# Kernel tuning notes

Measured on AMD Instinct MI355X. Metric: run time of the kernel, lower is better.

## Reference

```python
import jax, jax.numpy as jnp
import numpy as np

N_NODES = 50000
N_EDGES = 800000
IN_C = 128
HID = 128
OUT_C = 64
N_GRAPHS = 256


def setup_inputs() -> dict:
    key = jax.random.key(0)
    ks = jax.random.split(key, 12)
    x = jax.random.normal(ks[0], (N_NODES, IN_C), dtype=jnp.float32)
    edge_index = jax.random.randint(ks[1], (2, N_EDGES), 0, N_NODES, dtype=jnp.int32)
    batch = jnp.sort(jax.random.randint(ks[2], (N_NODES,), 0, N_GRAPHS, dtype=jnp.int32))
    def lin(k, fan_in, fan_out):
        bound = 1.0 / np.sqrt(fan_in)
        kw, kb = jax.random.split(k)
        W = jax.random.uniform(kw, (fan_in, fan_out), minval=-bound, maxval=bound, dtype=jnp.float32)
        b = jax.random.uniform(kb, (fan_out,), minval=-bound, maxval=bound, dtype=jnp.float32)
        return W, b
    W1a, b1a = lin(ks[3], IN_C, HID)
    W1b, b1b = lin(ks[4], HID, HID)
    W2a, b2a = lin(ks[5], HID, HID)
    W2b, b2b = lin(ks[6], HID, HID)
    Wl, bl = lin(ks[7], HID, OUT_C)
    return {"x": x, "edge_index": edge_index, "batch": batch,
            "W1a": W1a, "b1a": b1a, "W1b": W1b, "b1b": b1b,
            "W2a": W2a, "b2a": b2a, "W2b": W2b, "b2b": b2b,
            "Wl": Wl, "bl": bl}


def gin_conv(x, edge_index, Wa, ba, Wb, bb):
    # GINConv with eps=0: h_i = MLP(x_i + sum_{j->i} x_j)
    src, dst = edge_index[0], edge_index[1]
    agg = jax.ops.segment_sum(x[src], dst, num_segments=x.shape[0])  # [N, d]
    h = x + agg
    h = jax.nn.relu(h @ Wa + ba) @ Wb + bb
    return h


def reference(x, edge_index, batch, W1a, b1a, W1b, b1b, W2a, b2a, W2b, b2b, Wl, bl):
    h = gin_conv(x, edge_index, W1a, b1a, W1b, b1b)
    h = gin_conv(h, edge_index, W2a, b2a, W2b, b2b)
    # global mean pool over graphs in the batch
    sums = jax.ops.segment_sum(h, batch, num_segments=N_GRAPHS)          # [G, HID]
    cnts = jax.ops.segment_sum(jnp.ones((h.shape[0],), h.dtype), batch, num_segments=N_GRAPHS)
    pooled = sums / jnp.maximum(cnts, 1.0)[:, None]
    return pooled @ Wl + bl  # [G, OUT_C]
```

## Files before the change

kernel.cpp:

```cpp
#include <hip/hip_runtime.h>

constexpr int N  = 50000;
constexpr int E  = 800000;
constexpr int C  = 128;
constexpr int G  = 256;
constexpr int OC = 64;
constexpr int D  = 64;

constexpr int NBUCK = 196;
constexpr int BCAP  = 5120;
constexpr int EB = (E + 4095) / 4096;
constexpr int WB = 256;
constexpr int XB = (N * C / 8 + 255) / 256;

typedef __attribute__((ext_vector_type(8))) short short8;
typedef __attribute__((ext_vector_type(4))) float f32x4;
typedef __attribute__((ext_vector_type(2))) float f32x2;

__device__ __forceinline__ unsigned int au(float f) { return __float_as_uint(f); }

__device__ __forceinline__ unsigned short f2bf(float f) {
    unsigned int u = au(f);
    u += 0x7fffu + ((u >> 16) & 1u);
    return (unsigned short)(u >> 16);
}
__device__ __forceinline__ unsigned int pack_bf16(float lo, float hi) {
    return ((au(hi) + 0x8000u) & 0xFFFF0000u) | ((au(lo) + 0x8000u) >> 16);
}

__device__ __forceinline__ void acc16(f32x2* a, uint4 v) {
    a[0] += __builtin_amdgcn_cvt_pk_f32_fp8((int)v.x, false);
    a[1] += __builtin_amdgcn_cvt_pk_f32_fp8((int)v.x, true);
    a[2] += __builtin_amdgcn_cvt_pk_f32_fp8((int)v.y, false);
    a[3] += __builtin_amdgcn_cvt_pk_f32_fp8((int)v.y, true);
    a[4] += __builtin_amdgcn_cvt_pk_f32_fp8((int)v.z, false);
    a[5] += __builtin_amdgcn_cvt_pk_f32_fp8((int)v.z, true);
    a[6] += __builtin_amdgcn_cvt_pk_f32_fp8((int)v.w, false);
    a[7] += __builtin_amdgcn_cvt_pk_f32_fp8((int)v.w, true);
}
__device__ __forceinline__ void set16(f32x2* a, uint4 v) {
    a[0] = __builtin_amdgcn_cvt_pk_f32_fp8((int)v.x, false);
    a[1] = __builtin_amdgcn_cvt_pk_f32_fp8((int)v.x, true);
    a[2] = __builtin_amdgcn_cvt_pk_f32_fp8((int)v.y, false);
    a[3] = __builtin_amdgcn_cvt_pk_f32_fp8((int)v.y, true);
    a[4] = __builtin_amdgcn_cvt_pk_f32_fp8((int)v.z, false);
    a[5] = __builtin_amdgcn_cvt_pk_f32_fp8((int)v.z, true);
    a[6] = __builtin_amdgcn_cvt_pk_f32_fp8((int)v.w, false);
    a[7] = __builtin_amdgcn_cvt_pk_f32_fp8((int)v.w, true);
}


__global__ __launch_bounds__(256) void build_prep_kernel(const int* __restrict__ src,
                                                         const int* __restrict__ dst,
                                                         int* __restrict__ bcount,
                                                         unsigned int* __restrict__ bucketbuf,
                                                         const float* __restrict__ W1a,
                                                         const float* __restrict__ W1b,
                                                         const float* __restrict__ W2a,
                                                         const float* __restrict__ W2b,
                                                         const float* __restrict__ x,
                                                         unsigned short* __restrict__ wt,
                                                         unsigned int* __restrict__ x8) {
    int b = blockIdx.x;
    if (b < EB) {
        __shared__ int lcount[NBUCK];
        __shared__ int lbase[NBUCK];
        __shared__ int lcur[NBUCK];
        int tid = threadIdx.x;
        for (int i = tid; i < NBUCK; i += 256) { lcount[i] = 0; lcur[i] = 0; }
        __syncthreads();
        int e0 = b * 4096;
        int sv[16], dv[16];
#pragma unroll
        for (int i = 0; i < 16; ++i) {
            int e = e0 + i * 256 + tid;
            if (e < E) {
                sv[i] = src[e];
                dv[i] = dst[e];
                atomicAdd(&lcount[dv[i] >> 8], 1);
            } else {
                dv[i] = -1;
            }
        }
        __syncthreads();
        if (tid < NBUCK) {
            int c = lcount[tid];
            lbase[tid] = (c > 0) ? atomicAdd(&bcount[tid], c) : 0;
        }
        __syncthreads();
#pragma unroll
        for (int i = 0; i < 16; ++i) {
            if (dv[i] >= 0) {
                int bk = dv[i] >> 8;
                int pos = lbase[bk] + atomicAdd(&lcur[bk], 1);
                if (pos < BCAP)
                    bucketbuf[(size_t)bk * BCAP + pos] =
                        ((unsigned int)sv[i] << 16) | (unsigned int)(dv[i] & 255);
            }
        }
    } else if (b < EB + WB) {
        const float* Ws[4] = {W1a, W1b, W2a, W2b};
        int idx = (b - EB) * 256 + threadIdx.x;
        int which = idx >> 14;
        int el    = idx & 16383;
        int n = el >> 7, k = el & 127;
        wt[idx] = f2bf(Ws[which][k * 128 + n]);
    } else {
        int idx = (b - EB - WB) * 256 + threadIdx.x;
        const float4* x4 = (const float4*)x;
        float4 v0 = x4[idx * 2];
        float4 v1 = x4[idx * 2 + 1];
        unsigned int lo = 0, hi = 0;
        lo = (unsigned int)__builtin_amdgcn_cvt_pk_fp8_f32(v0.x, v0.y, (int)lo, false);
        lo = (unsigned int)__builtin_amdgcn_cvt_pk_fp8_f32(v0.z, v0.w, (int)lo, true);
        hi = (unsigned int)__builtin_amdgcn_cvt_pk_fp8_f32(v1.x, v1.y, (int)hi, false);
        hi = (unsigned int)__builtin_amdgcn_cvt_pk_fp8_f32(v1.z, v1.w, (int)hi, true);
        ((uint2*)x8)[idx] = make_uint2(lo, hi);
    }
}


__global__ __launch_bounds__(256) void bucket_fill_kernel(const int* __restrict__ bcount,
                                                          const unsigned int* __restrict__ bucketbuf,
                                                          unsigned short* __restrict__ ell,
                                                          int* __restrict__ deg) {
    __shared__ int lcur[256];
    int b = blockIdx.x;
    int tid = threadIdx.x;
    lcur[tid] = 0;
    __syncthreads();
    int cnt = min(bcount[b], BCAP);
    const unsigned int* buf = bucketbuf + (size_t)b * BCAP;
    int nbase = b << 8;
    for (int i = tid; i < cnt; i += 256) {
        unsigned int e = buf[i];
        int dlow = (int)(e & 255u);
        int s = (int)(e >> 16);
        int p = atomicAdd(&lcur[dlow], 1);
        if (p < D) ell[(size_t)p * N + nbase + dlow] = (unsigned short)s;
    }
    __syncthreads();
    int node = nbase + tid;
    if (node < N) deg[node] = lcur[tid];
}


__global__ __launch_bounds__(256) void aggregate_kernel(const unsigned char* __restrict__ Fg,
                                                        const int* __restrict__ deg,
                                                        const unsigned short* __restrict__ ell,
                                                        unsigned short* __restrict__ Y) {
    int grp = threadIdx.x >> 3;
    int l   = threadIdx.x & 7;
    int n = blockIdx.x * 32 + grp;
    if (n >= N) return;
    const uint4* F16 = (const uint4*)Fg;
    f32x2 a[8];
    int dg = min(deg[n], D);
    const unsigned short* ecol = ell + n;
    set16(a, F16[(size_t)n * 8 + l]);
    int j = 0;
    if (dg >= 8) {
        int i0 = ecol[0];
        int i1 = ecol[(size_t)1 * N];
        int i2 = ecol[(size_t)2 * N];
        int i3 = ecol[(size_t)3 * N];
        int i4 = ecol[(size_t)4 * N];
        int i5 = ecol[(size_t)5 * N];
        int i6 = ecol[(size_t)6 * N];
        int i7 = ecol[(size_t)7 * N];
        uint4 v0 = F16[(size_t)i0 * 8 + l];
        uint4 v1 = F16[(size_t)i1 * 8 + l];
        uint4 v2 = F16[(size_t)i2 * 8 + l];
        uint4 v3 = F16[(size_t)i3 * 8 + l];
        uint4 v4 = F16[(size_t)i4 * 8 + l];
        uint4 v5 = F16[(size_t)i5 * 8 + l];
        uint4 v6 = F16[(size_t)i6 * 8 + l];
        uint4 v7 = F16[(size_t)i7 * 8 + l];
        for (j = 8; j + 8 <= dg; j += 8) {
            int t0 = ecol[(size_t)(j + 0) * N];
            int t1 = ecol[(size_t)(j + 1) * N];
            int t2 = ecol[(size_t)(j + 2) * N];
            int t3 = ecol[(size_t)(j + 3) * N];
            int t4 = ecol[(size_t)(j + 4) * N];
            int t5 = ecol[(size_t)(j + 5) * N];
            int t6 = ecol[(size_t)(j + 6) * N];
            int t7 = ecol[(size_t)(j + 7) * N];
            uint4 w0 = F16[(size_t)t0 * 8 + l];
            uint4 w1 = F16[(size_t)t1 * 8 + l];
            uint4 w2 = F16[(size_t)t2 * 8 + l];
            uint4 w3 = F16[(size_t)t3 * 8 + l];
            uint4 w4 = F16[(size_t)t4 * 8 + l];
            uint4 w5 = F16[(size_t)t5 * 8 + l];
            uint4 w6 = F16[(size_t)t6 * 8 + l];
            uint4 w7 = F16[(size_t)t7 * 8 + l];
            acc16(a, v0); acc16(a, v1); acc16(a, v2); acc16(a, v3);
            acc16(a, v4); acc16(a, v5); acc16(a, v6); acc16(a, v7);
            v0 = w0; v1 = w1; v2 = w2; v3 = w3;
            v4 = w4; v5 = w5; v6 = w6; v7 = w7;
        }
        acc16(a, v0); acc16(a, v1); acc16(a, v2); acc16(a, v3);
        acc16(a, v4); acc16(a, v5); acc16(a, v6); acc16(a, v7);
    }
    for (; j < dg; ++j) {
        uint4 v = F16[(size_t)ecol[(size_t)j * N] * 8 + l];
        acc16(a, v);
    }
    uint4 o0, o1;
    o0.x = pack_bf16(a[0].x, a[0].y); o0.y = pack_bf16(a[1].x, a[1].y);
    o0.z = pack_bf16(a[2].x, a[2].y); o0.w = pack_bf16(a[3].x, a[3].y);
    o1.x = pack_bf16(a[4].x, a[4].y); o1.y = pack_bf16(a[5].x, a[5].y);
    o1.z = pack_bf16(a[6].x, a[6].y); o1.w = pack_bf16(a[7].x, a[7].y);
    uint4* yp = (uint4*)(Y + (size_t)n * 128 + l * 16);
    yp[0] = o0;
    yp[1] = o1;
}


__global__ __launch_bounds__(256) void mlp_kernel(const unsigned short* __restrict__ Xg,
                                                  const unsigned short* __restrict__ WaT,
                                                  const float* __restrict__ ba,
                                                  const unsigned short* __restrict__ WbT,
                                                  const float* __restrict__ bb,
                                                  unsigned char* __restrict__ Hg8,
                                                  unsigned short* __restrict__ Hgb,
                                                  int outFp8) {
    constexpr int LD = 136;
    __shared__ short Xl[64 * LD];
    __shared__ short Wl[128 * LD];
    int tid  = threadIdx.x;
    int lane = tid & 63;
    int wave = tid >> 6;
    int row0 = blockIdx.x * 64;

    const short8* Xg8 = (const short8*)(Xg + (size_t)row0 * 128);
#pragma unroll
    for (int i = tid; i < 1024; i += 256) {
        int r = i >> 4, c = i & 15;
        *((short8*)(Xl + r * LD) + c) = Xg8[i];
    }
    const short8* Wa8 = (const short8*)WaT;
#pragma unroll
    for (int i = tid; i < 2048; i += 256) {
        int r = i >> 4, c = i & 15;
        *((short8*)(Wl + r * LD) + c) = Wa8[i];
    }

    int mw = wave >> 1, nw = wave & 1;
    int lid = lane & 15, quad = lane >> 4;

    f32x4 acc[2][4];
#pragma unroll
    for (int nt = 0; nt < 4; ++nt) {
        float b = ba[nw * 64 + nt * 16 + lid];
        acc[0][nt] = (f32x4){b, b, b, b};
        acc[1][nt] = (f32x4){b, b, b, b};
    }
    __syncthreads();

#pragma unroll
    for (int ks = 0; ks < 4; ++ks) {
        short8 a0 = *(const short8*)(Xl + (mw * 32 + lid) * LD + ks * 32 + quad * 8);
        short8 a1 = *(const short8*)(Xl + (mw * 32 + 16 + lid) * LD + ks * 32 + quad * 8);
#pragma unroll
        for (int nt = 0; nt < 4; ++nt) {
            short8 bf = *(const short8*)(Wl + (nw * 64 + nt * 16 + lid) * LD + ks * 32 + quad * 8);
            acc[0][nt] = __builtin_amdgcn_mfma_f32_16x16x32_bf16(a0, bf, acc[0][nt], 0, 0, 0);
            acc[1][nt] = __builtin_amdgcn_mfma_f32_16x16x32_bf16(a1, bf, acc[1][nt], 0, 0, 0);
        }
    }
    __syncthreads();

#pragma unroll
    for (int mt = 0; mt < 2; ++mt) {
#pragma unroll
        for (int nt = 0; nt < 4; ++nt) {
            int mbase = mw * 32 + mt * 16 + quad * 4;
            int n = nw * 64 + nt * 16 + lid;
            f32x4 v = acc[mt][nt];
#pragma unroll
            for (int r = 0; r < 4; ++r)
                Xl[(mbase + r) * LD + n] = (short)f2bf(fmaxf(v[r], 0.f));
        }
    }
    const short8* Wb8 = (const short8*)WbT;
#pragma unroll
    for (int i = tid; i < 2048; i += 256) {
        int r = i >> 4, c = i & 15;
        *((short8*)(Wl + r * LD) + c) = Wb8[i];
    }
    f32x4 acc2[2][4];
#pragma unroll
    for (int nt = 0; nt < 4; ++nt) {
        float b = bb[nw * 64 + nt * 16 + lid];
        acc2[0][nt] = (f32x4){b, b, b, b};
        acc2[1][nt] = (f32x4){b, b, b, b};
    }
    __syncthreads();

#pragma unroll
    for (int ks = 0; ks < 4; ++ks) {
        short8 a0 = *(const short8*)(Xl + (mw * 32 + lid) * LD + ks * 32 + quad * 8);
        short8 a1 = *(const short8*)(Xl + (mw * 32 + 16 + lid) * LD + ks * 32 + quad * 8);
#pragma unroll
        for (int nt = 0; nt < 4; ++nt) {
            short8 bf = *(const short8*)(Wl + (nw * 64 + nt * 16 + lid) * LD + ks * 32 + quad * 8);
            acc2[0][nt] = __builtin_amdgcn_mfma_f32_16x16x32_bf16(a0, bf, acc2[0][nt], 0, 0, 0);
            acc2[1][nt] = __builtin_amdgcn_mfma_f32_16x16x32_bf16(a1, bf, acc2[1][nt], 0, 0, 0);
        }
    }

#pragma unroll
    for (int mt = 0; mt < 2; ++mt) {
#pragma unroll
        for (int nt = 0; nt < 4; ++nt) {
            int mbase = row0 + mw * 32 + mt * 16 + quad * 4;
            int n = nw * 64 + nt * 16 + lid;
            f32x4 v = acc2[mt][nt];
            if (outFp8) {
#pragma unroll
                for (int r = 0; r < 4; ++r) {
                    int row = mbase + r;
                    if (row < N) {
                        unsigned int p = (unsigned int)__builtin_amdgcn_cvt_pk_fp8_f32(v[r], 0.f, 0, false);
                        Hg8[(size_t)row * 128 + n] = (unsigned char)(p & 0xFF);
                    }
                }
            } else {
#pragma unroll
                for (int r = 0; r < 4; ++r) {
                    int row = mbase + r;
                    if (row < N) Hgb[(size_t)row * 128 + n] = f2bf(v[r]);
                }
            }
        }
    }
}


__global__ __launch_bounds__(256) void pool_partial_kernel(const unsigned short* __restrict__ H,
                                                           const int* __restrict__ batch,
                                                           float* __restrict__ gsum,
                                                           int* __restrict__ gcnt) {
    int tid = threadIdx.x;
    int w = tid >> 6;
    int l = tid & 63;
    int r0 = blockIdx.x * 64 + w * 16;
    if (r0 >= N) return;
    int rend = min(r0 + 16, N);
    const unsigned int* H2 = (const unsigned int*)H;
    int curg = batch[r0];
    int runstart = r0;
    float a0 = 0.f, a1 = 0.f;
    for (int r = r0; r < rend; ++r) {
        int g = batch[r];
        if (g != curg) {
            atomicAdd(&gsum[curg * C + 2 * l], a0);
            atomicAdd(&gsum[curg * C + 2 * l + 1], a1);
            if (l == 0) atomicAdd(&gcnt[curg], r - runstart);
            curg = g; runstart = r; a0 = 0.f; a1 = 0.f;
        }
        unsigned int v = H2[(size_t)r * 64 + l];
        a0 += __uint_as_float((v & 0xffffu) << 16);
        a1 += __uint_as_float(v & 0xffff0000u);
    }
    atomicAdd(&gsum[curg * C + 2 * l], a0);
    atomicAdd(&gsum[curg * C + 2 * l + 1], a1);
    if (l == 0) atomicAdd(&gcnt[curg], rend - runstart);
}


__global__ __launch_bounds__(64) void head_kernel(const float* __restrict__ gsum,
                                                  const int* __restrict__ gcnt,
                                                  const float* __restrict__ Wl,
                                                  const float* __restrict__ bl,
                                                  float* __restrict__ out) {
    int g = blockIdx.x;
    int t = threadIdx.x;
    __shared__ float pooled[C];
    float inv = 1.0f / (float)max(gcnt[g], 1);
    pooled[t]      = gsum[g * C + t] * inv;
    pooled[t + 64] = gsum[g * C + 64 + t] * inv;
    __syncthreads();
    float o = bl[t];
#pragma unroll 4
    for (int k = 0; k < C; ++k) o += pooled[k] * Wl[k * OC + t];
    out[g * OC + t] = o;
}


extern "C" void kernel_launch(void* const* d_in, const int* in_sizes, int n_in,
                              void* d_out, int out_size, void* d_ws, size_t ws_size,
                              hipStream_t stream) {
    const float* x    = (const float*)d_in[0];
    const int*   ei   = (const int*)d_in[1];
    const int*   bat  = (const int*)d_in[2];
    const float* W1a  = (const float*)d_in[3];
    const float* b1a  = (const float*)d_in[4];
    const float* W1b  = (const float*)d_in[5];
    const float* b1b  = (const float*)d_in[6];
    const float* W2a  = (const float*)d_in[7];
    const float* b2a  = (const float*)d_in[8];
    const float* W2b  = (const float*)d_in[9];
    const float* b2b  = (const float*)d_in[10];
    const float* Wl   = (const float*)d_in[11];
    const float* bl   = (const float*)d_in[12];
    float*       out  = (float*)d_out;

    float* gsum    = (float*)d_ws;
    int*   gcnt    = (int*)(gsum + G * C);
    int*   bcount  = gcnt + G;
    int*   deg     = bcount + NBUCK;
    unsigned int* bucketbuf = (unsigned int*)(deg + N);
    unsigned short* ell = (unsigned short*)(bucketbuf + (size_t)NBUCK * BCAP);
    unsigned short* wt  = ell + (size_t)N * D;
    unsigned char*  x8  = (unsigned char*)(wt + 4 * 16384);
    unsigned char*  h8  = x8 + (size_t)N * 128;
    unsigned short* y   = (unsigned short*)(h8 + (size_t)N * 128);
    unsigned short* hb  = y + (size_t)(N + 64) * 128;

    const unsigned short* wt1a = wt;
    const unsigned short* wt1b = wt + 16384;
    const unsigned short* wt2a = wt + 2 * 16384;
    const unsigned short* wt2b = wt + 3 * 16384;

    const int* src = ei;
    const int* dst = ei + E;

    hipMemsetAsync(gsum, 0, (size_t)(G * C + G + NBUCK) * sizeof(int), stream);

    build_prep_kernel<<<EB + WB + XB, 256, 0, stream>>>(src, dst, bcount, bucketbuf,
                                                        W1a, W1b, W2a, W2b, x,
                                                        wt, (unsigned int*)x8);
    bucket_fill_kernel<<<NBUCK, 256, 0, stream>>>(bcount, bucketbuf, ell, deg);

    int ab = (N + 31) / 32;
    int mb = (N + 63) / 64;

    aggregate_kernel<<<ab, 256, 0, stream>>>(x8, deg, ell, y);
    mlp_kernel<<<mb, 256, 0, stream>>>(y, wt1a, b1a, wt1b, b1b, h8, nullptr, 1);

    aggregate_kernel<<<ab, 256, 0, stream>>>(h8, deg, ell, y);
    mlp_kernel<<<mb, 256, 0, stream>>>(y, wt2a, b2a, wt2b, b2b, nullptr, hb, 0);

    pool_partial_kernel<<<mb, 256, 0, stream>>>(hb, bat, gsum, gcnt);
    head_kernel<<<G, 64, 0, stream>>>(gsum, gcnt, Wl, bl, out);
}
```

Measured before the change: 222.1 us.

## Fuse aggregation, MLP and mean-pool partial sums into one conv kernel

Merges the gather-sum aggregation into the MLP kernel so each block aggregates its 64 rows straight into shared memory, removing the bf16 intermediate round trip through global memory and two launches. The second conv's epilogue accumulates pooled sums with atomics directly instead of writing hidden states, and graph counts move into the prep kernel via a shared-memory histogram. The cost is lower occupancy and latency hiding for the gather phase, since it now shares a block with large LDS tiles, and more global atomics in the epilogue.

```diff
diff --git a/kernel.cpp b/kernel.cpp
--- a/kernel.cpp
+++ b/kernel.cpp
@@ -12,6 +12,7 @@
 constexpr int EB = (E + 4095) / 4096;
 constexpr int WB = 256;
 constexpr int XB = (N * C / 8 + 255) / 256;
+constexpr int GB = (N + 255) / 256;
 
 typedef __attribute__((ext_vector_type(8))) short short8;
 typedef __attribute__((ext_vector_type(4))) float f32x4;
@@ -60,7 +61,9 @@
                                                          const float* __restrict__ W2b,
                                                          const float* __restrict__ x,
                                                          unsigned short* __restrict__ wt,
-                                                         unsigned int* __restrict__ x8) {
+                                                         unsigned int* __restrict__ x8,
+                                                         const int* __restrict__ batch,
+                                                         int* __restrict__ gcnt) {
     int b = blockIdx.x;
     if (b < EB) {
         __shared__ int lcount[NBUCK];
@@ -105,7 +108,7 @@
         int el    = idx & 16383;
         int n = el >> 7, k = el & 127;
         wt[idx] = f2bf(Ws[which][k * 128 + n]);
-    } else {
+    } else if (b < EB + WB + XB) {
         int idx = (b - EB - WB) * 256 + threadIdx.x;
         const float4* x4 = (const float4*)x;
         float4 v0 = x4[idx * 2];
@@ -116,6 +119,16 @@
         hi = (unsigned int)__builtin_amdgcn_cvt_pk_fp8_f32(v1.x, v1.y, (int)hi, false);
         hi = (unsigned int)__builtin_amdgcn_cvt_pk_fp8_f32(v1.z, v1.w, (int)hi, true);
         ((uint2*)x8)[idx] = make_uint2(lo, hi);
+    } else {
+        __shared__ int h[G];
+        int tid = threadIdx.x;
+        h[tid] = 0;
+        __syncthreads();
+        int i = (b - EB - WB - XB) * 256 + tid;
+        if (i < N) atomicAdd(&h[batch[i]], 1);
+        __syncthreads();
+        int c = h[tid];
+        if (c > 0) atomicAdd(&gcnt[tid], c);
     }
 }
 
@@ -145,85 +158,17 @@
 }
 
 
-__global__ __launch_bounds__(256) void aggregate_kernel(const unsigned char* __restrict__ Fg,
-                                                        const int* __restrict__ deg,
-                                                        const unsigned short* __restrict__ ell,
-                                                        unsigned short* __restrict__ Y) {
-    int grp = threadIdx.x >> 3;
-    int l   = threadIdx.x & 7;
-    int n = blockIdx.x * 32 + grp;
-    if (n >= N) return;
-    const uint4* F16 = (const uint4*)Fg;
-    f32x2 a[8];
-    int dg = min(deg[n], D);
-    const unsigned short* ecol = ell + n;
-    set16(a, F16[(size_t)n * 8 + l]);
-    int j = 0;
-    if (dg >= 8) {
-        int i0 = ecol[0];
-        int i1 = ecol[(size_t)1 * N];
-        int i2 = ecol[(size_t)2 * N];
-        int i3 = ecol[(size_t)3 * N];
-        int i4 = ecol[(size_t)4 * N];
-        int i5 = ecol[(size_t)5 * N];
-        int i6 = ecol[(size_t)6 * N];
-        int i7 = ecol[(size_t)7 * N];
-        uint4 v0 = F16[(size_t)i0 * 8 + l];
-        uint4 v1 = F16[(size_t)i1 * 8 + l];
-        uint4 v2 = F16[(size_t)i2 * 8 + l];
-        uint4 v3 = F16[(size_t)i3 * 8 + l];
-        uint4 v4 = F16[(size_t)i4 * 8 + l];
-        uint4 v5 = F16[(size_t)i5 * 8 + l];
-        uint4 v6 = F16[(size_t)i6 * 8 + l];
-        uint4 v7 = F16[(size_t)i7 * 8 + l];
-        for (j = 8; j + 8 <= dg; j += 8) {
-            int t0 = ecol[(size_t)(j + 0) * N];
-            int t1 = ecol[(size_t)(j + 1) * N];
-            int t2 = ecol[(size_t)(j + 2) * N];
-            int t3 = ecol[(size_t)(j + 3) * N];
-            int t4 = ecol[(size_t)(j + 4) * N];
-            int t5 = ecol[(size_t)(j + 5) * N];
-            int t6 = ecol[(size_t)(j + 6) * N];
-            int t7 = ecol[(size_t)(j + 7) * N];
-            uint4 w0 = F16[(size_t)t0 * 8 + l];
-            uint4 w1 = F16[(size_t)t1 * 8 + l];
-            uint4 w2 = F16[(size_t)t2 * 8 + l];
-            uint4 w3 = F16[(size_t)t3 * 8 + l];
-            uint4 w4 = F16[(size_t)t4 * 8 + l];
-            uint4 w5 = F16[(size_t)t5 * 8 + l];
-            uint4 w6 = F16[(size_t)t6 * 8 + l];
-            uint4 w7 = F16[(size_t)t7 * 8 + l];
-            acc16(a, v0); acc16(a, v1); acc16(a, v2); acc16(a, v3);
-            acc16(a, v4); acc16(a, v5); acc16(a, v6); acc16(a, v7);
-            v0 = w0; v1 = w1; v2 = w2; v3 = w3;
-            v4 = w4; v5 = w5; v6 = w6; v7 = w7;
-        }
-        acc16(a, v0); acc16(a, v1); acc16(a, v2); acc16(a, v3);
-        acc16(a, v4); acc16(a, v5); acc16(a, v6); acc16(a, v7);
-    }
-    for (; j < dg; ++j) {
-        uint4 v = F16[(size_t)ecol[(size_t)j * N] * 8 + l];
-        acc16(a, v);
-    }
-    uint4 o0, o1;
-    o0.x = pack_bf16(a[0].x, a[0].y); o0.y = pack_bf16(a[1].x, a[1].y);
-    o0.z = pack_bf16(a[2].x, a[2].y); o0.w = pack_bf16(a[3].x, a[3].y);
-    o1.x = pack_bf16(a[4].x, a[4].y); o1.y = pack_bf16(a[5].x, a[5].y);
-    o1.z = pack_bf16(a[6].x, a[6].y); o1.w = pack_bf16(a[7].x, a[7].y);
-    uint4* yp = (uint4*)(Y + (size_t)n * 128 + l * 16);
-    yp[0] = o0;
-    yp[1] = o1;
-}
-
-
-__global__ __launch_bounds__(256) void mlp_kernel(const unsigned short* __restrict__ Xg,
-                                                  const unsigned short* __restrict__ WaT,
-                                                  const float* __restrict__ ba,
-                                                  const unsigned short* __restrict__ WbT,
-                                                  const float* __restrict__ bb,
-                                                  unsigned char* __restrict__ Hg8,
-                                                  unsigned short* __restrict__ Hgb,
-                                                  int outFp8) {
+__global__ __launch_bounds__(256) void conv_kernel(const unsigned char* __restrict__ Fg,
+                                                   const int* __restrict__ deg,
+                                                   const unsigned short* __restrict__ ell,
+                                                   const unsigned short* __restrict__ WaT,
+                                                   const float* __restrict__ ba,
+                                                   const unsigned short* __restrict__ WbT,
+                                                   const float* __restrict__ bb,
+                                                   unsigned char* __restrict__ Hg8,
+                                                   const int* __restrict__ batch,
+                                                   float* __restrict__ gsum,
+                                                   int outFp8) {
     constexpr int LD = 136;
     __shared__ short Xl[64 * LD];
     __shared__ short Wl[128 * LD];
@@ -232,17 +177,86 @@
     int wave = tid >> 6;
     int row0 = blockIdx.x * 64;
 
-    const short8* Xg8 = (const short8*)(Xg + (size_t)row0 * 128);
-#pragma unroll
-    for (int i = tid; i < 1024; i += 256) {
-        int r = i >> 4, c = i & 15;
-        *((short8*)(Xl + r * LD) + c) = Xg8[i];
-    }
     const short8* Wa8 = (const short8*)WaT;
 #pragma unroll
     for (int i = tid; i < 2048; i += 256) {
         int r = i >> 4, c = i & 15;
         *((short8*)(Wl + r * LD) + c) = Wa8[i];
+    }
+
+    {
+        int grp = tid >> 3;
+        int l   = tid & 7;
+        const uint4* F16 = (const uint4*)Fg;
+#pragma unroll 1
+        for (int pass = 0; pass < 2; ++pass) {
+            int lr = pass * 32 + grp;
+            int n  = row0 + lr;
+            f32x2 a[8];
+            if (n < N) {
+                int dg = min(deg[n], D);
+                const unsigned short* ecol = ell + n;
+                set16(a, F16[(size_t)n * 8 + l]);
+                int j = 0;
+                if (dg >= 8) {
+                    int i0 = ecol[0];
+                    int i1 = ecol[(size_t)1 * N];
+                    int i2 = ecol[(size_t)2 * N];
+                    int i3 = ecol[(size_t)3 * N];
+                    int i4 = ecol[(size_t)4 * N];
+                    int i5 = ecol[(size_t)5 * N];
+                    int i6 = ecol[(size_t)6 * N];
+                    int i7 = ecol[(size_t)7 * N];
+                    uint4 v0 = F16[(size_t)i0 * 8 + l];
+                    uint4 v1 = F16[(size_t)i1 * 8 + l];
+                    uint4 v2 = F16[(size_t)i2 * 8 + l];
+                    uint4 v3 = F16[(size_t)i3 * 8 + l];
+                    uint4 v4 = F16[(size_t)i4 * 8 + l];
+                    uint4 v5 = F16[(size_t)i5 * 8 + l];
+                    uint4 v6 = F16[(size_t)i6 * 8 + l];
+                    uint4 v7 = F16[(size_t)i7 * 8 + l];
+                    for (j = 8; j + 8 <= dg; j += 8) {
+                        int t0 = ecol[(size_t)(j + 0) * N];
+                        int t1 = ecol[(size_t)(j + 1) * N];
+                        int t2 = ecol[(size_t)(j + 2) * N];
+                        int t3 = ecol[(size_t)(j + 3) * N];
+                        int t4 = ecol[(size_t)(j + 4) * N];
+                        int t5 = ecol[(size_t)(j + 5) * N];
+                        int t6 = ecol[(size_t)(j + 6) * N];
+                        int t7 = ecol[(size_t)(j + 7) * N];
+                        uint4 w0 = F16[(size_t)t0 * 8 + l];
+                        uint4 w1 = F16[(size_t)t1 * 8 + l];
+                        uint4 w2 = F16[(size_t)t2 * 8 + l];
+                        uint4 w3 = F16[(size_t)t3 * 8 + l];
+                        uint4 w4 = F16[(size_t)t4 * 8 + l];
+                        uint4 w5 = F16[(size_t)t5 * 8 + l];
+                        uint4 w6 = F16[(size_t)t6 * 8 + l];
+                        uint4 w7 = F16[(size_t)t7 * 8 + l];
+                        acc16(a, v0); acc16(a, v1); acc16(a, v2); acc16(a, v3);
+                        acc16(a, v4); acc16(a, v5); acc16(a, v6); acc16(a, v7);
+                        v0 = w0; v1 = w1; v2 = w2; v3 = w3;
+                        v4 = w4; v5 = w5; v6 = w6; v7 = w7;
+                    }
+                    acc16(a, v0); acc16(a, v1); acc16(a, v2); acc16(a, v3);
+                    acc16(a, v4); acc16(a, v5); acc16(a, v6); acc16(a, v7);
+                }
+                for (; j < dg; ++j) {
+                    uint4 v = F16[(size_t)ecol[(size_t)j * N] * 8 + l];
+                    acc16(a, v);
+                }
+            } else {
+#pragma unroll
+                for (int q = 0; q < 8; ++q) a[q] = (f32x2){0.f, 0.f};
+            }
+            uint4 o0, o1;
+            o0.x = pack_bf16(a[0].x, a[0].y); o0.y = pack_bf16(a[1].x, a[1].y);
+            o0.z = pack_bf16(a[2].x, a[2].y); o0.w = pack_bf16(a[3].x, a[3].y);
+            o1.x = pack_bf16(a[4].x, a[4].y); o1.y = pack_bf16(a[5].x, a[5].y);
+            o1.z = pack_bf16(a[6].x, a[6].y); o1.w = pack_bf16(a[7].x, a[7].y);
+            uint4* xp = (uint4*)(Xl + lr * LD + l * 16);
+            xp[0] = o0;
+            xp[1] = o1;
+        }
     }
 
     int mw = wave >> 1, nw = wave & 1;
@@ -326,46 +340,25 @@
                     }
                 }
             } else {
+                int gprev = -1;
+                float s = 0.f;
 #pragma unroll
                 for (int r = 0; r < 4; ++r) {
                     int row = mbase + r;
-                    if (row < N) Hgb[(size_t)row * 128 + n] = f2bf(v[r]);
+                    if (row < N) {
+                        int g = batch[row];
+                        if (g != gprev) {
+                            if (gprev >= 0) atomicAdd(&gsum[gprev * C + n], s);
+                            gprev = g;
+                            s = 0.f;
+                        }
+                        s += v[r];
+                    }
                 }
+                if (gprev >= 0) atomicAdd(&gsum[gprev * C + n], s);
             }
         }
     }
-}
-
-
-__global__ __launch_bounds__(256) void pool_partial_kernel(const unsigned short* __restrict__ H,
-                                                           const int* __restrict__ batch,
-                                                           float* __restrict__ gsum,
-                                                           int* __restrict__ gcnt) {
-    int tid = threadIdx.x;
-    int w = tid >> 6;
-    int l = tid & 63;
-    int r0 = blockIdx.x * 64 + w * 16;
-    if (r0 >= N) return;
-    int rend = min(r0 + 16, N);
-    const unsigned int* H2 = (const unsigned int*)H;
-    int curg = batch[r0];
-    int runstart = r0;
-    float a0 = 0.f, a1 = 0.f;
-    for (int r = r0; r < rend; ++r) {
-        int g = batch[r];
-        if (g != curg) {
-            atomicAdd(&gsum[curg * C + 2 * l], a0);
-            atomicAdd(&gsum[curg * C + 2 * l + 1], a1);
-            if (l == 0) atomicAdd(&gcnt[curg], r - runstart);
-            curg = g; runstart = r; a0 = 0.f; a1 = 0.f;
-        }
-        unsigned int v = H2[(size_t)r * 64 + l];
-        a0 += __uint_as_float((v & 0xffffu) << 16);
-        a1 += __uint_as_float(v & 0xffff0000u);
-    }
-    atomicAdd(&gsum[curg * C + 2 * l], a0);
-    atomicAdd(&gsum[curg * C + 2 * l + 1], a1);
-    if (l == 0) atomicAdd(&gcnt[curg], rend - runstart);
 }
 
 
@@ -415,8 +408,6 @@
     unsigned short* wt  = ell + (size_t)N * D;
     unsigned char*  x8  = (unsigned char*)(wt + 4 * 16384);
     unsigned char*  h8  = x8 + (size_t)N * 128;
-    unsigned short* y   = (unsigned short*)(h8 + (size_t)N * 128);
-    unsigned short* hb  = y + (size_t)(N + 64) * 128;
 
     const unsigned short* wt1a = wt;
     const unsigned short* wt1b = wt + 16384;
@@ -428,20 +419,18 @@
 
     hipMemsetAsync(gsum, 0, (size_t)(G * C + G + NBUCK) * sizeof(int), stream);
 
-    build_prep_kernel<<<EB + WB + XB, 256, 0, stream>>>(src, dst, bcount, bucketbuf,
-                                                        W1a, W1b, W2a, W2b, x,
-                                                        wt, (unsigned int*)x8);
+    build_prep_kernel<<<EB + WB + XB + GB, 256, 0, stream>>>(src, dst, bcount, bucketbuf,
+                                                             W1a, W1b, W2a, W2b, x,
+                                                             wt, (unsigned int*)x8,
+                                                             bat, gcnt);
     bucket_fill_kernel<<<NBUCK, 256, 0, stream>>>(bcount, bucketbuf, ell, deg);
 
-    int ab = (N + 31) / 32;
     int mb = (N + 63) / 64;
 
-    aggregate_kernel<<<ab, 256, 0, stream>>>(x8, deg, ell, y);
-    mlp_kernel<<<mb, 256, 0, stream>>>(y, wt1a, b1a, wt1b, b1b, h8, nullptr, 1);
-
-    aggregate_kernel<<<ab, 256, 0, stream>>>(h8, deg, ell, y);
-    mlp_kernel<<<mb, 256, 0, stream>>>(y, wt2a, b2a, wt2b, b2b, nullptr, hb, 0);
-
-    pool_partial_kernel<<<mb, 256, 0, stream>>>(hb, bat, gsum, gcnt);
+    conv_kernel<<<mb, 256, 0, stream>>>(x8, deg, ell, wt1a, b1a, wt1b, b1b,
+                                        h8, nullptr, nullptr, 1);
+    conv_kernel<<<mb, 256, 0, stream>>>(h8, deg, ell, wt2a, b2a, wt2b, b2b,
+                                        nullptr, bat, gsum, 0);
+
     head_kernel<<<G, 64, 0, stream>>>(gsum, gcnt, Wl, bl, out);
 }
```

Measured after the change: 228.0 us. +2.7%, slower.
